# Kernel tuning notes

Measured on AMD Instinct MI355X. Metric: run time of the kernel, lower is better.

The kernel has to match this reference:

```python
import jax, jax.numpy as jnp
import numpy as np

PS = 32
NUM_ANG_BINS = 36


def circular_gauss_kernel(kernlen):
    # CircularGaussKernel from the HardNet repo (norm=True, circ_zeros=False)
    half = kernlen / 2.0
    r2 = half * half
    sigma2 = 0.9 * r2
    x = np.linspace(-half, half, kernlen)
    xv, yv = np.meshgrid(x, x, indexing='xy')
    d2 = xv ** 2 + yv ** 2
    k = np.exp(-d2 / sigma2)
    k = k / np.sum(k)
    return jnp.asarray(k, dtype=jnp.float32)


def setup_inputs() -> dict:
    key = jax.random.key(0)
    x = jax.random.uniform(key, (65536, 1, PS, PS), dtype=jnp.float32)
    return {"x": x}


def reference(x):
    B = x.shape[0]
    gk = 10.0 * circular_gauss_kernel(PS)  # [PS, PS]

    # gx: Conv2d kernel [[0.5, 0, -0.5]] with replicate pad (1,1,0,0)
    xp = jnp.pad(x, ((0, 0), (0, 0), (0, 0), (1, 1)), mode='edge')
    gx = 0.5 * (xp[..., :-2] - xp[..., 2:])
    # gy: Conv2d kernel [[0.5],[0],[-0.5]] with replicate pad (0,0,1,1)
    yp = jnp.pad(x, ((0, 0), (0, 0), (1, 1), (0, 0)), mode='edge')
    gy = 0.5 * (yp[:, :, :-2, :] - yp[:, :, 2:, :])

    mag = jnp.sqrt(gx * gx + gy * gy + 1e-10) * gk  # gk broadcasts over [B,1,PS,PS]
    ori = jnp.arctan2(gy, gx)

    o_big = NUM_ANG_BINS * (ori + jnp.pi) / (2.0 * jnp.pi)
    bo0 = jnp.floor(o_big)
    wo1 = o_big - bo0
    bo0 = (bo0 % NUM_ANG_BINS).astype(jnp.int32)
    wo0 = (1.0 - wo1) * mag  # note: upper-bin weight wo1*mag is dropped, as in original

    # histogram via per-patch scatter-add (replaces 36 masked full-tensor scans)
    bins_flat = bo0.reshape(B, -1)  # [B, PS*PS]
    w_flat = wo0.reshape(B, -1)
    hist = jax.vmap(lambda w, b: jax.ops.segment_sum(w, b, num_segments=NUM_ANG_BINS))(
        w_flat, bins_flat) / float(PS * PS)  # adaptive_avg_pool2d -> mean

    # Conv1d angular smoothing, kernel [0.33,0.34,0.33], zero padding=1
    hp = jnp.pad(hist, ((0, 0), (1, 1)))
    sm = 0.33 * hp[:, :-2] + 0.34 * hp[:, 1:-1] + 0.33 * hp[:, 2:]

    idx = jnp.argmax(sm, axis=1)
    angle = -(2.0 * jnp.pi * idx.astype(x.dtype) / NUM_ANG_BINS - jnp.pi)
    return angle
```

## Files before the change

kernel.cpp:

```cpp
#include <hip/hip_runtime.h>

#define PS 32
#define NPIX (PS * PS)
#define NB 36
#define WPB 4
#define HCOL 64
#define HWORDS (NB * HCOL)

__global__ __launch_bounds__(256) void gk_init_kernel(float* __restrict__ gk10) {
    __shared__ double red[256];
    const int tid = threadIdx.x;
    const double delta = 32.0 / 31.0;
    const double sigma2 = 0.9 * 256.0;

    double kv[4];
    double s = 0.0;
#pragma unroll
    for (int j = 0; j < 4; ++j) {
        int p = tid * 4 + j;
        int r = p >> 5, c = p & 31;
        double xr = (r == 31) ? 16.0 : ((double)r * delta + (-16.0));
        double xc = (c == 31) ? 16.0 : ((double)c * delta + (-16.0));
        double d2 = xc * xc + xr * xr;
        kv[j] = exp(-d2 / sigma2);
        s += kv[j];
    }
    red[tid] = s;
    __syncthreads();
    for (int off = 128; off > 0; off >>= 1) {
        if (tid < off) red[tid] += red[tid + off];
        __syncthreads();
    }
    double sum = red[0];
#pragma unroll
    for (int j = 0; j < 4; ++j) {
        int p = tid * 4 + j;
        gk10[p] = __fmul_rn(10.0f, (float)(kv[j] / sum));
    }
}

__device__ __attribute__((noinline))
void fix_pixel(float lv, float rv, float uv, float dv, float gk, float* col) {
    const float PI_F    = 3.14159265358979323846f;
    const float TWOPI_F = 6.28318530717958647692f;
    float gx = __fmul_rn(0.5f, __fsub_rn(lv, rv));
    float gy = __fmul_rn(0.5f, __fsub_rn(uv, dv));
    float s2 = __fadd_rn(__fadd_rn(__fmul_rn(gx, gx), __fmul_rn(gy, gy)), 1e-10f);
    float mag = __fmul_rn(__fsqrt_rn(s2), gk);

    float ori  = (float)atan2((double)gy, (double)gx);
    float obig = __fdiv_rn(__fmul_rn(36.0f, __fadd_rn(ori, PI_F)), TWOPI_F);
    float bo0f = floorf(obig);
    float wo1  = __fsub_rn(obig, bo0f);
    int bo = (int)bo0f;
    if (bo >= NB) bo -= NB;
    float wo0 = __fmul_rn(__fsub_rn(1.0f, wo1), mag);
    col[bo * HCOL] += wo0;
}

__global__ __launch_bounds__(256) void orient_kernel(const float* __restrict__ x,
                                                     const float* __restrict__ gk10,
                                                     float* __restrict__ out) {
    const float PI_F    = 3.14159265358979323846f;
    const float TWOPI_F = 6.28318530717958647692f;

    __shared__ __align__(16) float lds[WPB][HWORDS];

    const int tid = threadIdx.x;
    const int w = tid >> 6;
    const int l = tid & 63;
    const int patch = blockIdx.x * WPB + w;

    float* rw = lds[w];

    const int r  = l >> 3;
    const int c0 = (l & 7) << 2;

    const float4* src = reinterpret_cast<const float4*>(x + (size_t)patch * NPIX);
    float4 ld[4], gkq[4];
#pragma unroll
    for (int k = 0; k < 4; ++k) ld[k] = src[k * 64 + l];
#pragma unroll
    for (int k = 0; k < 4; ++k)
        gkq[k] = *reinterpret_cast<const float4*>(&gk10[(k * 8 + r) * PS + c0]);

    float4* dst = reinterpret_cast<float4*>(rw);
#pragma unroll
    for (int k = 0; k < 4; ++k) dst[k * 64 + l] = ld[k];
    asm volatile("s_waitcnt lgkmcnt(0)" ::: "memory");

    float4 up[4], dn[4];
    float  lsc[4], rsc[4];
#pragma unroll
    for (int k = 0; k < 4; ++k) {
        const int row = k * 8 + r;
        const int rowOff = row << 5;
        const int upOff  = ((row == 0)  ? 0  : (row - 1)) << 5;
        const int dnOff  = ((row == 31) ? 31 : (row + 1)) << 5;
        up[k]  = *reinterpret_cast<const float4*>(&rw[upOff + c0]);
        dn[k]  = *reinterpret_cast<const float4*>(&rw[dnOff + c0]);
        lsc[k] = rw[rowOff + ((c0 == 0) ? 0 : (c0 - 1))];
        rsc[k] = rw[rowOff + ((c0 + 4 > 31) ? 31 : (c0 + 4))];
    }
    asm volatile("s_waitcnt lgkmcnt(0)" ::: "memory");

#pragma unroll
    for (int p = 0; p < 9; ++p)
        dst[p * 64 + l] = make_float4(0.0f, 0.0f, 0.0f, 0.0f);
    asm volatile("s_waitcnt lgkmcnt(0)" ::: "memory");

    unsigned int badbits = 0;
    float* mycol = rw + l;
#pragma unroll
    for (int k = 0; k < 4; ++k) {
        float sv[4]  = {ld[k].x, ld[k].y, ld[k].z, ld[k].w};
        float uv[4]  = {up[k].x, up[k].y, up[k].z, up[k].w};
        float dv[4]  = {dn[k].x, dn[k].y, dn[k].z, dn[k].w};
        float gk4[4] = {gkq[k].x, gkq[k].y, gkq[k].z, gkq[k].w};
        float lv[4]  = {lsc[k], sv[0], sv[1], sv[2]};
        float rv[4]  = {sv[1],  sv[2], sv[3], rsc[k]};

#pragma unroll
        for (int j = 0; j < 4; ++j) {
            const int i = k * 4 + j;
            float gx = __fmul_rn(0.5f, __fsub_rn(lv[j], rv[j]));
            float gy = __fmul_rn(0.5f, __fsub_rn(uv[j], dv[j]));
            float s2 = __fadd_rn(__fadd_rn(__fmul_rn(gx, gx), __fmul_rn(gy, gy)), 1e-10f);
            float mag = __fmul_rn(__fsqrt_rn(s2), gk4[j]);

            float ax = fabsf(gx), ay = fabsf(gy);
            float mn = fminf(ax, ay), mx = fmaxf(ax, ay);
            float rr = mn * __builtin_amdgcn_rcpf(mx);
            rr = (mx > 0.0f) ? rr : 0.0f;
            float t  = rr * rr;
            float u = 0.00282363896258175373077393f;
            u = fmaf(u, t, -0.0159569028764963150024414f);
            u = fmaf(u, t,  0.0425049886107444763183594f);
            u = fmaf(u, t, -0.0748900920152664184570312f);
            u = fmaf(u, t,  0.106347933411598205566406f);
            u = fmaf(u, t, -0.142027363181114196777344f);
            u = fmaf(u, t,  0.199926957488059997558594f);
            u = fmaf(u, t, -0.333331018686294555664062f);
            float at = fmaf(rr * t, u, rr);

            bool c1 = ay > ax;
            bool c2 = gx < 0.0f;
            bool c3 = gy < 0.0f;
            float S  = c1 ? -1.0f : 1.0f;
            float Cb = c1 ? 27.0f : 18.0f;
            S  = c2 ? -S : S;
            Cb = c2 ? __fsub_rn(54.0f, Cb) : Cb;
            S  = c3 ? -S : S;
            Cb = c3 ? __fsub_rn(36.0f, Cb) : Cb;
            float obig = fmaf(at * S, 5.72957795130823208768f, Cb);
            float bo0f = floorf(obig);
            float wo1  = __fsub_rn(obig, bo0f);

            bool bad = (wo1 < 2e-5f) | (wo1 > 1.0f - 2e-5f);
            if (!bad) {
                int bo = (int)bo0f;
                if (bo >= NB) bo -= NB;
                float wo0 = __fmul_rn(__fsub_rn(1.0f, wo1), mag);
                mycol[bo * HCOL] += wo0;
            } else {
                badbits |= (1u << i);
            }
        }
    }

    if (__ballot(badbits != 0)) {
#pragma unroll
        for (int k = 0; k < 4; ++k) {
            float sv[4]  = {ld[k].x, ld[k].y, ld[k].z, ld[k].w};
            float uv[4]  = {up[k].x, up[k].y, up[k].z, up[k].w};
            float dv[4]  = {dn[k].x, dn[k].y, dn[k].z, dn[k].w};
            float gk4[4] = {gkq[k].x, gkq[k].y, gkq[k].z, gkq[k].w};
            float lv[4]  = {lsc[k], sv[0], sv[1], sv[2]};
            float rv[4]  = {sv[1],  sv[2], sv[3], rsc[k]};
#pragma unroll
            for (int j = 0; j < 4; ++j) {
                if (badbits & (1u << (k * 4 + j)))
                    fix_pixel(lv[j], rv[j], uv[j], dv[j], gk4[j], mycol);
            }
        }
    }
    asm volatile("s_waitcnt lgkmcnt(0)" ::: "memory");

    float hval = 0.0f;
    if (l < NB) {
        const float4* row4 = reinterpret_cast<const float4*>(rw + l * HCOL);
        float tot = 0.0f;
#pragma unroll
        for (int k = 0; k < 16; ++k) {
            float4 a = row4[(k + l) & 15];
            tot += ((a.x + a.y) + (a.z + a.w));
        }
        hval = __fmul_rn(tot, 1.0f / 1024.0f);
    }

    float hm = __shfl_up(hval, 1, 64);
    if (l == 0) hm = 0.0f;
    float hp = __shfl_down(hval, 1, 64);
    float sm = 0.0f;
    if (l < NB) {
        sm = __fadd_rn(__fadd_rn(__fmul_rn(0.33f, hm), __fmul_rn(0.34f, hval)),
                       __fmul_rn(0.33f, hp));
    }

    unsigned long long key =
        (l < NB) ? ((((unsigned long long)__float_as_uint(sm)) << 6) |
                    (unsigned long long)(63 - l))
                 : 0ull;
#pragma unroll
    for (int off = 32; off > 0; off >>= 1) {
        unsigned long long o = __shfl_xor(key, off, 64);
        key = (o > key) ? o : key;
    }

    if (l == 0) {
        int bi = 63 - (int)(key & 63);
        float t2 = __fdiv_rn(__fmul_rn(TWOPI_F, (float)bi), 36.0f);
        out[patch] = __fsub_rn(PI_F, t2);
    }
}

extern "C" void kernel_launch(void* const* d_in, const int* in_sizes, int n_in,
                              void* d_out, int out_size, void* d_ws, size_t ws_size,
                              hipStream_t stream) {
    const float* x = (const float*)d_in[0];
    float* out = (float*)d_out;
    float* gk10 = (float*)d_ws;

    const int B = in_sizes[0] / NPIX;

    gk_init_kernel<<<1, 256, 0, stream>>>(gk10);
    orient_kernel<<<B / WPB, 256, 0, stream>>>(x, gk10, out);
}
```

Before: 119.3 us.

## Use 4x4 pixel tiles per lane with shuffle halo exchange instead of LDS staging

Each lane now loads a 4x4 pixel tile directly from global memory rather than four rows of four pixels. The up/down/left/right halo values come from cross-lane shuffles, which removes the round trip of staging the patch in shared memory and reading neighbours back. The histogram column reduction switches from float4 to float2 reads. The trade-offs are strided 16-byte global loads (each row of 4 floats sits 128 bytes apart) and extra shuffle instructions.

New measurement: 123.3 us. 3.4% more time.

```diff
diff --git a/kernel.cpp b/kernel.cpp
--- a/kernel.cpp
+++ b/kernel.cpp
@@ -64,69 +64,88 @@
     const float PI_F    = 3.14159265358979323846f;
     const float TWOPI_F = 6.28318530717958647692f;
 
-    __shared__ __align__(16) float lds[WPB][HWORDS];
+    __shared__ __align__(16) float hist[WPB][HWORDS];
 
     const int tid = threadIdx.x;
     const int w = tid >> 6;
     const int l = tid & 63;
     const int patch = blockIdx.x * WPB + w;
 
-    float* rw = lds[w];
-
-    const int r  = l >> 3;
-    const int c0 = (l & 7) << 2;
-
-    const float4* src = reinterpret_cast<const float4*>(x + (size_t)patch * NPIX);
-    float4 ld[4], gkq[4];
-#pragma unroll
-    for (int k = 0; k < 4; ++k) ld[k] = src[k * 64 + l];
-#pragma unroll
-    for (int k = 0; k < 4; ++k)
-        gkq[k] = *reinterpret_cast<const float4*>(&gk10[(k * 8 + r) * PS + c0]);
-
-    float4* dst = reinterpret_cast<float4*>(rw);
-#pragma unroll
-    for (int k = 0; k < 4; ++k) dst[k * 64 + l] = ld[k];
-    asm volatile("s_waitcnt lgkmcnt(0)" ::: "memory");
-
-    float4 up[4], dn[4];
-    float  lsc[4], rsc[4];
-#pragma unroll
-    for (int k = 0; k < 4; ++k) {
-        const int row = k * 8 + r;
-        const int rowOff = row << 5;
-        const int upOff  = ((row == 0)  ? 0  : (row - 1)) << 5;
-        const int dnOff  = ((row == 31) ? 31 : (row + 1)) << 5;
-        up[k]  = *reinterpret_cast<const float4*>(&rw[upOff + c0]);
-        dn[k]  = *reinterpret_cast<const float4*>(&rw[dnOff + c0]);
-        lsc[k] = rw[rowOff + ((c0 == 0) ? 0 : (c0 - 1))];
-        rsc[k] = rw[rowOff + ((c0 + 4 > 31) ? 31 : (c0 + 4))];
-    }
-    asm volatile("s_waitcnt lgkmcnt(0)" ::: "memory");
-
-#pragma unroll
-    for (int p = 0; p < 9; ++p)
-        dst[p * 64 + l] = make_float4(0.0f, 0.0f, 0.0f, 0.0f);
-    asm volatile("s_waitcnt lgkmcnt(0)" ::: "memory");
+    float* hw = hist[w];
+
+    const int sr = l >> 3;
+    const int sc = l & 7;
+
+    const float* xb = x + (size_t)patch * NPIX + (sr * 4) * PS + sc * 4;
+    const float* gb = gk10 + (sr * 4) * PS + sc * 4;
+    float4 sq[4], gq[4];
+#pragma unroll
+    for (int k = 0; k < 4; ++k) {
+        sq[k] = *reinterpret_cast<const float4*>(xb + k * PS);
+        gq[k] = *reinterpret_cast<const float4*>(gb + k * PS);
+    }
+
+    {
+        float4 z4 = make_float4(0.0f, 0.0f, 0.0f, 0.0f);
+        float4* hz = reinterpret_cast<float4*>(hw);
+#pragma unroll
+        for (int p = 0; p < 9; ++p) hz[p * 64 + l] = z4;
+    }
+
+    float s[4][4], g[4][4];
+#pragma unroll
+    for (int k = 0; k < 4; ++k) {
+        s[k][0] = sq[k].x; s[k][1] = sq[k].y; s[k][2] = sq[k].z; s[k][3] = sq[k].w;
+        g[k][0] = gq[k].x; g[k][1] = gq[k].y; g[k][2] = gq[k].z; g[k][3] = gq[k].w;
+    }
+
+    const int upL = (sr > 0) ? (l - 8) : l;
+    const int dnL = (sr < 7) ? (l + 8) : l;
+    const int lfL = (sc > 0) ? (l - 1) : l;
+    const int rtL = (sc < 7) ? (l + 1) : l;
+    float Uh[4], Dh[4], Lh[4], Rh[4];
+#pragma unroll
+    for (int j = 0; j < 4; ++j) {
+        Uh[j] = __shfl(s[3][j], upL, 64);
+        Dh[j] = __shfl(s[0][j], dnL, 64);
+    }
+#pragma unroll
+    for (int k = 0; k < 4; ++k) {
+        Lh[k] = __shfl(s[k][3], lfL, 64);
+        Rh[k] = __shfl(s[k][0], rtL, 64);
+    }
+    if (sr == 0) {
+#pragma unroll
+        for (int j = 0; j < 4; ++j) Uh[j] = s[0][j];
+    }
+    if (sr == 7) {
+#pragma unroll
+        for (int j = 0; j < 4; ++j) Dh[j] = s[3][j];
+    }
+    if (sc == 0) {
+#pragma unroll
+        for (int k = 0; k < 4; ++k) Lh[k] = s[k][0];
+    }
+    if (sc == 7) {
+#pragma unroll
+        for (int k = 0; k < 4; ++k) Rh[k] = s[k][3];
+    }
 
     unsigned int badbits = 0;
-    float* mycol = rw + l;
-#pragma unroll
-    for (int k = 0; k < 4; ++k) {
-        float sv[4]  = {ld[k].x, ld[k].y, ld[k].z, ld[k].w};
-        float uv[4]  = {up[k].x, up[k].y, up[k].z, up[k].w};
-        float dv[4]  = {dn[k].x, dn[k].y, dn[k].z, dn[k].w};
-        float gk4[4] = {gkq[k].x, gkq[k].y, gkq[k].z, gkq[k].w};
-        float lv[4]  = {lsc[k], sv[0], sv[1], sv[2]};
-        float rv[4]  = {sv[1],  sv[2], sv[3], rsc[k]};
-
+    float* mycol = hw + l;
+#pragma unroll
+    for (int k = 0; k < 4; ++k) {
 #pragma unroll
         for (int j = 0; j < 4; ++j) {
-            const int i = k * 4 + j;
-            float gx = __fmul_rn(0.5f, __fsub_rn(lv[j], rv[j]));
-            float gy = __fmul_rn(0.5f, __fsub_rn(uv[j], dv[j]));
+            float lv = (j == 0) ? Lh[k] : s[k][j - 1];
+            float rv = (j == 3) ? Rh[k] : s[k][j + 1];
+            float uv = (k == 0) ? Uh[j] : s[k - 1][j];
+            float dv = (k == 3) ? Dh[j] : s[k + 1][j];
+
+            float gx = __fmul_rn(0.5f, __fsub_rn(lv, rv));
+            float gy = __fmul_rn(0.5f, __fsub_rn(uv, dv));
             float s2 = __fadd_rn(__fadd_rn(__fmul_rn(gx, gx), __fmul_rn(gy, gy)), 1e-10f);
-            float mag = __fmul_rn(__fsqrt_rn(s2), gk4[j]);
+            float mag = __fmul_rn(__fsqrt_rn(s2), g[k][j]);
 
             float ax = fabsf(gx), ay = fabsf(gy);
             float mn = fminf(ax, ay), mx = fmaxf(ax, ay);
@@ -163,7 +182,7 @@
                 float wo0 = __fmul_rn(__fsub_rn(1.0f, wo1), mag);
                 mycol[bo * HCOL] += wo0;
             } else {
-                badbits |= (1u << i);
+                badbits |= (1u << (k * 4 + j));
             }
         }
     }
@@ -171,16 +190,15 @@
     if (__ballot(badbits != 0)) {
 #pragma unroll
         for (int k = 0; k < 4; ++k) {
-            float sv[4]  = {ld[k].x, ld[k].y, ld[k].z, ld[k].w};
-            float uv[4]  = {up[k].x, up[k].y, up[k].z, up[k].w};
-            float dv[4]  = {dn[k].x, dn[k].y, dn[k].z, dn[k].w};
-            float gk4[4] = {gkq[k].x, gkq[k].y, gkq[k].z, gkq[k].w};
-            float lv[4]  = {lsc[k], sv[0], sv[1], sv[2]};
-            float rv[4]  = {sv[1],  sv[2], sv[3], rsc[k]};
 #pragma unroll
             for (int j = 0; j < 4; ++j) {
-                if (badbits & (1u << (k * 4 + j)))
-                    fix_pixel(lv[j], rv[j], uv[j], dv[j], gk4[j], mycol);
+                if (badbits & (1u << (k * 4 + j))) {
+                    float lv = (j == 0) ? Lh[k] : s[k][j - 1];
+                    float rv = (j == 3) ? Rh[k] : s[k][j + 1];
+                    float uv = (k == 0) ? Uh[j] : s[k - 1][j];
+                    float dv = (k == 3) ? Dh[j] : s[k + 1][j];
+                    fix_pixel(lv, rv, uv, dv, g[k][j], mycol);
+                }
             }
         }
     }
@@ -188,12 +206,12 @@
 
     float hval = 0.0f;
     if (l < NB) {
-        const float4* row4 = reinterpret_cast<const float4*>(rw + l * HCOL);
+        const float2* row2 = reinterpret_cast<const float2*>(hw + l * HCOL);
         float tot = 0.0f;
 #pragma unroll
-        for (int k = 0; k < 16; ++k) {
-            float4 a = row4[(k + l) & 15];
-            tot += ((a.x + a.y) + (a.z + a.w));
+        for (int k = 0; k < 32; ++k) {
+            float2 a = row2[(k + l) & 31];
+            tot += (a.x + a.y);
         }
         hval = __fmul_rn(tot, 1.0f / 1024.0f);
     }
```
